# Kernel optimization log

Hardware: AMD Instinct MI355X
Metric: run time of the kernel (lower is better)

## Reference

```python
import jax, jax.numpy as jnp
import numpy as np

# Mamba2 hyperparams fixed by MambaBlock.__init__ (d_model=512, d_state=128, d_conv=4, expand=4, headdim=64)
D_MODEL = 512
D_STATE = 128      # N
D_CONV = 4
EXPAND = 4
HEADDIM = 64       # P
D_INNER = EXPAND * D_MODEL            # 2048
NHEADS = D_INNER // HEADDIM           # 32
NGROUPS = 1
CONV_DIM = D_INNER + 2 * NGROUPS * D_STATE      # 2304 (x, B, C share the depthwise conv)
D_IN_PROJ = 2 * D_INNER + 2 * NGROUPS * D_STATE + NHEADS  # 4384 (z, xBC, dt)
EPS = 1e-5


def _mamba2(x, in_w, conv_w, conv_b, dt_bias, A_log, Dp, norm_w, out_w):
    """Faithful Mamba2 forward (ngroups=1). x: [B, L, d_model]."""
    Bsz, L, _ = x.shape
    zxbcdt = jnp.einsum('bld,pd->blp', x, in_w)  # in_proj (no bias)
    z, xBC, dt = jnp.split(zxbcdt, [D_INNER, D_INNER + CONV_DIM], axis=-1)
    # causal depthwise conv1d over xBC, kernel size D_CONV, then SiLU
    xp = jnp.pad(xBC, ((0, 0), (D_CONV - 1, 0), (0, 0)))
    xBC = sum(xp[:, k:k + L, :] * conv_w[:, k] for k in range(D_CONV)) + conv_b
    xBC = jax.nn.silu(xBC)
    xs, Bc, Cc = jnp.split(xBC, [D_INNER, D_INNER + D_STATE], axis=-1)
    xs = xs.reshape(Bsz, L, NHEADS, HEADDIM)          # [B,L,H,P]
    dt = jax.nn.softplus(dt + dt_bias)                 # [B,L,H]
    A = -jnp.exp(A_log)                                # [H]
    dA = jnp.exp(dt * A)                               # [B,L,H] discrete state decay

    def step(h, inp):
        dA_t, dt_t, x_t, B_t, C_t = inp  # [B,H],[B,H],[B,H,P],[B,N],[B,N]
        h = h * dA_t[:, :, None, None] + (dt_t[:, :, None] * x_t)[..., None] * B_t[:, None, None, :]
        y = jnp.einsum('bhpn,bn->bhp', h, C_t)
        return h, y

    h0 = jnp.zeros((Bsz, NHEADS, HEADDIM, D_STATE), x.dtype)
    inps = (dA.transpose(1, 0, 2), dt.transpose(1, 0, 2), xs.transpose(1, 0, 2, 3),
            Bc.transpose(1, 0, 2), Cc.transpose(1, 0, 2))
    _, ys = jax.lax.scan(step, h0, inps)               # [L,B,H,P]
    y = ys.transpose(1, 0, 2, 3) + Dp[None, None, :, None] * xs  # skip via D
    y = y.reshape(Bsz, L, D_INNER)
    # RMSNormGated (norm_before_gate=False): gate first, then RMSNorm
    y = y * jax.nn.silu(z)
    y = y * jax.lax.rsqrt(jnp.mean(y * y, axis=-1, keepdims=True) + EPS) * norm_w
    return jnp.einsum('bld,od->blo', y, out_w)         # out_proj (no bias)


def _make_params(key):
    ks = jax.random.split(key, 8)
    return dict(
        in_w=jax.random.normal(ks[0], (D_IN_PROJ, D_MODEL), jnp.float32) / np.sqrt(D_MODEL),
        conv_w=jax.random.normal(ks[1], (CONV_DIM, D_CONV), jnp.float32) * 0.2,
        conv_b=jax.random.normal(ks[2], (CONV_DIM,), jnp.float32) * 0.02,
        dt_bias=jax.random.normal(ks[3], (NHEADS,), jnp.float32) * 0.1,
        A_log=jnp.log(jax.random.uniform(ks[4], (NHEADS,), jnp.float32, 1.0, 16.0)),
        D=jnp.ones((NHEADS,), jnp.float32),
        norm_w=jnp.ones((D_INNER,), jnp.float32),
        out_w=jax.random.normal(ks[5], (D_MODEL, D_INNER), jnp.float32) / np.sqrt(D_INNER),
    )


def setup_inputs() -> dict:
    key = jax.random.key(0)
    k_in, k_f, k_b = jax.random.split(key, 3)
    x = jax.random.normal(k_in, (2, 2048, D_MODEL), jnp.float32)
    pf = _make_params(k_f)
    pb = _make_params(k_b)
    out = {'input': x}
    for n, v in pf.items():
        out['f_' + n] = v
    for n, v in pb.items():
        out['b_' + n] = v
    return out


def reference(input, f_in_w, f_conv_w, f_conv_b, f_dt_bias, f_A_log, f_D, f_norm_w, f_out_w,
              b_in_w, b_conv_w, b_conv_b, b_dt_bias, b_A_log, b_D, b_norm_w, b_out_w):
    fwd = _mamba2(input, f_in_w, f_conv_w, f_conv_b, f_dt_bias, f_A_log, f_D, f_norm_w, f_out_w)
    xb = jnp.flip(input, axis=1)
    bwd = _mamba2(xb, b_in_w, b_conv_w, b_conv_b, b_dt_bias, b_A_log, b_D, b_norm_w, b_out_w)
    bwd = jnp.flip(bwd, axis=1)
    return jnp.concatenate([fwd + input, bwd + input], axis=-1)
```

## Files before the change

### kernel.cpp

```cpp
#include <hip/hip_runtime.h>
#include <hip/hip_bf16.h>
#include <math.h>

#define L_SEQ   2048
#define M_ROWS  4096
#define DPROJ   4384
#define DPROJP  4480
#define NPROJ   4352
#define DINNER  2048
#define CONVDIM 2304
#define NST     128
#define NH      32
#define CHUNK   128
#define NCH     16
#define CTR     32
#define NTILE   (L_SEQ / CTR)
#define LOG2E   1.4426950408889634f

typedef __attribute__((ext_vector_type(8))) short short8;
typedef __attribute__((ext_vector_type(4))) float f32x4;
typedef unsigned short u16;

static __device__ __forceinline__ u16 bf16bits(float v) {
    __hip_bfloat16 t = __float2bfloat16(v);
    return *(u16*)&t;
}
static __device__ __forceinline__ float bits2f(u16 u) {
    return __uint_as_float((unsigned)u << 16);
}
static __device__ __forceinline__ int sidx(int row, int s) {
    return (row << 7) + ((((s >> 3) ^ (row & 7)) << 3) | (s & 7));
}
static __device__ __forceinline__ int sslot(int row, int ks) {
    return (row << 7) + ((ks ^ (row & 7)) << 3);
}
static __device__ __forceinline__ void gload16(const void* g, void* l) {
    __builtin_amdgcn_global_load_lds(
        (const __attribute__((address_space(1))) void*)g,
        (__attribute__((address_space(3))) void*)l, 16, 0, 0);
}

__global__ __launch_bounds__(256) void cvt_x_kernel(
    const float* __restrict__ x, u16* __restrict__ xbf)
{
    const int i = (blockIdx.x * 256 + threadIdx.x) * 4;
    const float4 v = *(const float4*)(x + i);
    xbf[i + 0] = bf16bits(v.x);
    xbf[i + 1] = bf16bits(v.y);
    xbf[i + 2] = bf16bits(v.z);
    xbf[i + 3] = bf16bits(v.w);
}

__global__ __launch_bounds__(256) void cvt_win_kernel(
    const float* __restrict__ w0, const float* __restrict__ w1,
    u16* __restrict__ dst)
{
    const int dir = blockIdx.y;
    const float* __restrict__ w = dir ? w1 : w0;
    u16* __restrict__ d = dst + (size_t)dir * NPROJ * 512;
    const int i = (blockIdx.x * 256 + threadIdx.x) * 4;
    const float4 v = *(const float4*)(w + i);
    d[i + 0] = bf16bits(v.x);
    d[i + 1] = bf16bits(v.y);
    d[i + 2] = bf16bits(v.z);
    d[i + 3] = bf16bits(v.w);
}

__global__ __launch_bounds__(256) void cvt_wout_kernel(
    const float* __restrict__ w0, const float* __restrict__ w1,
    u16* __restrict__ dst)
{
    const int dir = blockIdx.y;
    const float* __restrict__ w = dir ? w1 : w0;
    u16* __restrict__ d = dst + (size_t)dir * 512 * DINNER;
    const int i = (blockIdx.x * 256 + threadIdx.x) * 4;
    const float4 v = *(const float4*)(w + i);
    d[i + 0] = bf16bits(v.x);
    d[i + 1] = bf16bits(v.y);
    d[i + 2] = bf16bits(v.z);
    d[i + 3] = bf16bits(v.w);
}

__global__ __launch_bounds__(256) void gemm_mfma_in(
    const u16* __restrict__ A0, int lda,
    const u16* __restrict__ Bw, long long b_dir_off,
    u16* __restrict__ Cb, long long c_dir_off, int ldc,
    int K)
{
    const int dir = blockIdx.z;
    const int nwg  = gridDim.x * gridDim.y;
    const int flat = blockIdx.y * gridDim.x + blockIdx.x;
    const int q = nwg >> 3, r = nwg & 7;
    const int xcd = flat & 7, idx = flat >> 3;
    const int wg = (xcd < r) ? xcd * (q + 1) + idx
                             : r * (q + 1) + (xcd - r) * q + idx;
    const int m0 = (wg / gridDim.x) * 128;
    const int n0 = (wg % gridDim.x) * 128;

    const u16* __restrict__ A = A0;
    const u16* __restrict__ B = Bw + (size_t)dir * b_dir_off;

    __shared__ u16 Asl[128 * 64];
    __shared__ u16 Bsl[128 * 64];

    const int tid  = threadIdx.x;
    const int lane = tid & 63;
    const int wid  = tid >> 6;
    const int wr   = (wid >> 1) << 6;
    const int wc   = (wid & 1) << 6;
    const int l15  = lane & 15;
    const int l4   = lane >> 4;

    f32x4 acc[4][4];
#pragma unroll
    for (int m = 0; m < 4; ++m)
#pragma unroll
        for (int n = 0; n < 4; ++n) acc[m][n] = (f32x4)0.f;

    for (int k0 = 0; k0 < K; k0 += 64) {
        __syncthreads();
#pragma unroll
        for (int i = 0; i < 4; ++i) {
            const int c    = tid + (i << 8);
            const int row  = c >> 3;
            const int scol = ((c & 7) ^ (row & 7)) << 3;
            gload16(A + (size_t)(m0 + row) * lda + k0 + scol, (char*)Asl + (c << 4));
            gload16(B + (size_t)(n0 + row) * K   + k0 + scol, (char*)Bsl + (c << 4));
        }
        __syncthreads();

#pragma unroll
        for (int kh = 0; kh < 2; ++kh) {
            const int ks = (kh << 2) + l4;
            short8 a[4], b[4];
#pragma unroll
            for (int m = 0; m < 4; ++m) {
                const int R = wr + (m << 4) + l15;
                a[m] = *(const short8*)((const char*)Asl + (R << 7) + ((ks ^ (R & 7)) << 4));
            }
#pragma unroll
            for (int n = 0; n < 4; ++n) {
                const int R = wc + (n << 4) + l15;
                b[n] = *(const short8*)((const char*)Bsl + (R << 7) + ((ks ^ (R & 7)) << 4));
            }
#pragma unroll
            for (int m = 0; m < 4; ++m)
#pragma unroll
                for (int n = 0; n < 4; ++n)
                    acc[m][n] = __builtin_amdgcn_mfma_f32_16x16x32_bf16(
                        a[m], b[n], acc[m][n], 0, 0, 0);
        }
    }

#pragma unroll
    for (int m = 0; m < 4; ++m) {
        const int row0 = m0 + wr + (m << 4) + (l4 << 2);
#pragma unroll
        for (int n = 0; n < 4; ++n) {
            const int col = n0 + wc + (n << 4) + l15;
#pragma unroll
            for (int r2 = 0; r2 < 4; ++r2)
                Cb[(size_t)dir * c_dir_off + (size_t)(row0 + r2) * ldc + col] =
                    bf16bits(acc[m][n][r2]);
        }
    }
}

__global__ __launch_bounds__(256) void gemm_out_kernel(
    const u16* __restrict__ Azx,
    const u16* __restrict__ Bw,
    const float* __restrict__ x,
    float* __restrict__ out)
{
    const int dir = blockIdx.z;
    const int nwg  = gridDim.x * gridDim.y;
    const int flat = blockIdx.y * gridDim.x + blockIdx.x;
    const int q = nwg >> 3;
    const int xcd = flat & 7, idx = flat >> 3;
    const int wg = xcd * q + idx;
    const int m0 = (wg >> 3) * 128;
    const int n0 = (wg & 7) * 64;

    const u16* __restrict__ A = Azx + (size_t)dir * M_ROWS * DPROJP + DINNER;
    const u16* __restrict__ B = Bw + (size_t)dir * 512 * DINNER;

    __shared__ u16 Asl[128 * 64];
    __shared__ u16 Bsl[64 * 64];

    const int tid  = threadIdx.x;
    const int lane = tid & 63;
    const int wid  = tid >> 6;
    const int wr   = (wid >> 1) << 6;
    const int wc   = (wid & 1) << 5;
    const int l15  = lane & 15;
    const int l4   = lane >> 4;

    f32x4 acc[4][2];
#pragma unroll
    for (int m = 0; m < 4; ++m)
#pragma unroll
        for (int n = 0; n < 2; ++n) acc[m][n] = (f32x4)0.f;

    for (int k0 = 0; k0 < DINNER; k0 += 64) {
        __syncthreads();
#pragma unroll
        for (int i = 0; i < 4; ++i) {
            const int c    = tid + (i << 8);
            const int row  = c >> 3;
            const int scol = ((c & 7) ^ (row & 7)) << 3;
            gload16(A + (size_t)(m0 + row) * DPROJP + k0 + scol, (char*)Asl + (c << 4));
        }
#pragma unroll
        for (int i = 0; i < 2; ++i) {
            const int c    = tid + (i << 8);
            const int row  = c >> 3;
            const int scol = ((c & 7) ^ (row & 7)) << 3;
            gload16(B + (size_t)(n0 + row) * DINNER + k0 + scol, (char*)Bsl + (c << 4));
        }
        __syncthreads();

#pragma unroll
        for (int kh = 0; kh < 2; ++kh) {
            const int ks = (kh << 2) + l4;
            short8 a[4], b[2];
#pragma unroll
            for (int m = 0; m < 4; ++m) {
                const int R = wr + (m << 4) + l15;
                a[m] = *(const short8*)((const char*)Asl + (R << 7) + ((ks ^ (R & 7)) << 4));
            }
#pragma unroll
            for (int n = 0; n < 2; ++n) {
                const int R = wc + (n << 4) + l15;
                b[n] = *(const short8*)((const char*)Bsl + (R << 7) + ((ks ^ (R & 7)) << 4));
            }
#pragma unroll
            for (int m = 0; m < 4; ++m)
#pragma unroll
                for (int n = 0; n < 2; ++n)
                    acc[m][n] = __builtin_amdgcn_mfma_f32_16x16x32_bf16(
                        a[m], b[n], acc[m][n], 0, 0, 0);
        }
    }

#pragma unroll
    for (int m = 0; m < 4; ++m) {
        const int row0 = m0 + wr + (m << 4) + (l4 << 2);
#pragma unroll
        for (int n = 0; n < 2; ++n) {
            const int col = n0 + wc + (n << 4) + l15;
#pragma unroll
            for (int r2 = 0; r2 < 4; ++r2) {
                const float v = acc[m][n][r2] + x[(size_t)(row0 + r2) * 512 + col];
                out[(size_t)(row0 + r2) * 1024 + dir * 512 + col] = v;
            }
        }
    }
}

__global__ __launch_bounds__(256) void conv_kernel(
    const u16* __restrict__ zx,
    const float* __restrict__ cw0, const float* __restrict__ cw1,
    const float* __restrict__ cb0, const float* __restrict__ cb1,
    u16* __restrict__ xs, u16* __restrict__ Bbf, u16* __restrict__ Cbf)
{
    const int dir = blockIdx.z;
    const int c   = blockIdx.x * 256 + threadIdx.x;
    const int b   = blockIdx.y >> 6;
    const int r0  = (blockIdx.y & (NTILE - 1)) * CTR;

    const float* __restrict__ cw = dir ? cw1 : cw0;
    const float w0 = cw[c * 4 + 0], w1 = cw[c * 4 + 1];
    const float w2 = cw[c * 4 + 2], w3 = cw[c * 4 + 3];
    const float bias = (dir ? cb1 : cb0)[c];

    const u16* __restrict__ zcol = zx + (size_t)dir * M_ROWS * DPROJP
        + (size_t)(b * L_SEQ) * DPROJP + DINNER + c;
    const size_t obase = (size_t)(dir * M_ROWS + b * L_SEQ);

    auto emit = [&](int l, float acc) {
        const float s = acc / (1.f + expf(-acc));
        const size_t orow = obase + l;
        if (c < DINNER)            xs[orow * DINNER + c] = bf16bits(s);
        else if (c < DINNER + NST) Bbf[orow * NST + (c - DINNER)] = bf16bits(s);
        else                       Cbf[orow * NST + (c - DINNER - NST)] = bf16bits(s);
    };

    if (dir == 0) {
        float h0 = (r0 - 3 >= 0) ? bits2f(zcol[(size_t)(r0 - 3) * DPROJP]) : 0.f;
        float h1 = (r0 - 2 >= 0) ? bits2f(zcol[(size_t)(r0 - 2) * DPROJP]) : 0.f;
        float h2 = (r0 - 1 >= 0) ? bits2f(zcol[(size_t)(r0 - 1) * DPROJP]) : 0.f;
#pragma unroll 8
        for (int l = r0; l < r0 + CTR; ++l) {
            const float zl = bits2f(zcol[(size_t)l * DPROJP]);
            float acc = bias;
            acc = fmaf(w0, h0, acc);
            acc = fmaf(w1, h1, acc);
            acc = fmaf(w2, h2, acc);
            acc = fmaf(w3, zl, acc);
            emit(l, acc);
            h0 = h1; h1 = h2; h2 = zl;
        }
    } else {
        const int le = r0 + CTR - 1;
        float h1 = (le + 1 < L_SEQ) ? bits2f(zcol[(size_t)(le + 1) * DPROJP]) : 0.f;
        float h2 = (le + 2 < L_SEQ) ? bits2f(zcol[(size_t)(le + 2) * DPROJP]) : 0.f;
        float h3 = (le + 3 < L_SEQ) ? bits2f(zcol[(size_t)(le + 3) * DPROJP]) : 0.f;
#pragma unroll 8
        for (int l = le; l >= r0; --l) {
            const float zl = bits2f(zcol[(size_t)l * DPROJP]);
            float acc = bias;
            acc = fmaf(w3, zl, acc);
            acc = fmaf(w2, h1, acc);
            acc = fmaf(w1, h2, acc);
            acc = fmaf(w0, h3, acc);
            emit(l, acc);
            h3 = h2; h2 = h1; h1 = zl;
        }
    }
}

__global__ __launch_bounds__(512) void dt_kernel(
    const float* __restrict__ x,
    const float* __restrict__ inw0, const float* __restrict__ inw1,
    const float* __restrict__ dtbias0, const float* __restrict__ dtbias1,
    const float* __restrict__ Alog0, const float* __restrict__ Alog1,
    float* __restrict__ dtb, float* __restrict__ dta)
{
    const int dir = blockIdx.y;
    const int r0  = blockIdx.x * 64;
    const int tid = threadIdx.x;

    __shared__ float wT[512 * 32];
    __shared__ float sbias[NH], sa[NH];

    const float* __restrict__ w = (dir ? inw1 : inw0) + (size_t)(DINNER + CONVDIM) * 512;
    for (int i = tid; i < 4096; i += 512) {
        const int flat = i * 4;
        const int h = flat >> 9;
        const int k = flat & 511;
        const float4 v = *(const float4*)(w + flat);
        *(float4*)&wT[(k >> 2) * 128 + h * 4] = v;
    }
    if (tid < NH) {
        sbias[tid] = (dir ? dtbias1 : dtbias0)[tid];
        sa[tid] = -expf((dir ? Alog1 : Alog0)[tid]) * LOG2E;
    }
    __syncthreads();

    const int h  = tid & 31;
    const int rr = tid >> 5;
    const float bias = sbias[h];
    const float a = sa[h];

    for (int rp = 0; rp < 64; rp += 16) {
        const int row = r0 + rp + rr;
        const float4* __restrict__ xr = (const float4*)(x + (size_t)row * 512);
        float4 s4 = make_float4(0.f, 0.f, 0.f, 0.f);
#pragma unroll 8
        for (int k4 = 0; k4 < 128; ++k4) {
            const float4 xv = xr[k4];
            const float4 wv = *(const float4*)&wT[k4 * 128 + h * 4];
            s4.x = fmaf(xv.x, wv.x, s4.x);
            s4.y = fmaf(xv.y, wv.y, s4.y);
            s4.z = fmaf(xv.z, wv.z, s4.z);
            s4.w = fmaf(xv.w, wv.w, s4.w);
        }
        const float v = (s4.x + s4.y) + (s4.z + s4.w) + bias;
        const float sp = (v > 20.f) ? v : log1pf(expf(v));
        const size_t orow = (size_t)(dir * M_ROWS + row);
        dtb[orow * NH + h] = sp;
        dta[orow * NH + h] = sp * a;
    }
}

__global__ __launch_bounds__(256) void sraw_kernel(
    const u16* __restrict__ Bbf, const u16* __restrict__ Cbf,
    u16* __restrict__ Sraw)
{
    const int bx  = blockIdx.x;
    const int ch  = bx & (NCH - 1);
    const int db  = bx >> 4;
    const int dir = db >> 1, bb = db & 1;
    const int tid = threadIdx.x;
    const int wid = tid >> 6;
    const int lane = tid & 63;
    const int l15 = lane & 15, l4 = lane >> 4;
    const int t0  = ch * CHUNK;
    const size_t dbase = (size_t)(dir * M_ROWS + bb * L_SEQ);
    const size_t base  = ((size_t)bx) << 14;

    auto lidx = [&](int t) { return dir ? (L_SEQ - 1 - t) : t; };

    f32x4 accs[2][8];
#pragma unroll
    for (int m = 0; m < 2; ++m)
#pragma unroll
        for (int j = 0; j < 8; ++j) accs[m][j] = (f32x4)0.f;

    short8 af[2][4];
#pragma unroll
    for (int m = 0; m < 2; ++m) {
        const size_t crow = dbase + lidx(t0 + wid * 32 + m * 16 + l15);
#pragma unroll
        for (int kk = 0; kk < 4; ++kk)
            af[m][kk] = *(const short8*)(Cbf + crow * NST + kk * 32 + l4 * 8);
    }
#pragma unroll
    for (int j = 0; j < 8; ++j) {
        const size_t brow = dbase + lidx(t0 + j * 16 + l15);
        short8 bf_[4];
#pragma unroll
        for (int kk = 0; kk < 4; ++kk)
            bf_[kk] = *(const short8*)(Bbf + brow * NST + kk * 32 + l4 * 8);
#pragma unroll
        for (int m = 0; m < 2; ++m)
#pragma unroll
            for (int kk = 0; kk < 4; ++kk)
                accs[m][j] = __builtin_amdgcn_mfma_f32_16x16x32_bf16(
                    af[m][kk], bf_[kk], accs[m][j], 0, 0, 0);
    }

#pragma unroll
    for (int m = 0; m < 2; ++m)
#pragma unroll
        for (int j = 0; j < 8; ++j)
#pragma unroll
            for (int r = 0; r < 4; ++r) {
                const int t = wid * 32 + m * 16 + l4 * 4 + r;
                const int s = j * 16 + l15;
                Sraw[base + (size_t)t * 128 + s] = bf16bits(accs[m][j][r]);
            }
}

__global__ __launch_bounds__(512) void ssd_state_kernel(
    const u16* __restrict__ xs, const u16* __restrict__ Bbf,
    const float* __restrict__ dtb, const float* __restrict__ dta,
    u16* __restrict__ stateC, float* __restrict__ betac)
{
    const int bx  = blockIdx.x;
    const int ch  = bx & (NCH - 1);
    const int bh  = bx >> 4;
    const int dir = bh >> 6;
    const int bb  = (bh >> 5) & 1;
    const int h   = bh & 31;
    const int tid = threadIdx.x;
    const int wid = tid >> 6;
    const int lane = tid & 63;
    const int l15 = lane & 15;
    const int l4  = lane >> 4;
    const int t0  = ch * CHUNK;
    const size_t dbase = (size_t)(dir * M_ROWS + bb * L_SEQ);

    __shared__ u16 XT[64 * 128];
    __shared__ u16 WBT[128 * 128];
    __shared__ float scum[CHUNK];
    __shared__ float sdt[CHUNK];

    auto lidx = [&](int t) { return dir ? (L_SEQ - 1 - t) : t; };

    const int sP = tid >> 2;
    const size_t grow = dbase + lidx(t0 + sP);
    const int p0 = (tid & 3) * 16;
    const int n0 = (tid & 3) * 32;
    short8 xv[2], bv[4];
#pragma unroll
    for (int q = 0; q < 2; ++q)
        xv[q] = *(const short8*)(xs + grow * DINNER + h * 64 + p0 + q * 8);
#pragma unroll
    for (int q = 0; q < 4; ++q)
        bv[q] = *(const short8*)(Bbf + grow * NST + n0 + q * 8);

    if (tid >= 128 && tid < 256) {
        const int s = tid - 128;
        sdt[s] = dtb[(dbase + lidx(t0 + s)) * NH + h];
    }
    if (wid == 0) {
        float a0 = dta[(dbase + lidx(t0 + lane)) * NH + h];
        float a1 = dta[(dbase + lidx(t0 + 64 + lane)) * NH + h];
#pragma unroll
        for (int off = 1; off < 64; off <<= 1) {
            const float u0 = __shfl_up(a0, off);
            const float u1 = __shfl_up(a1, off);
            if (lane >= off) { a0 += u0; a1 += u1; }
        }
        a1 += __shfl(a0, 63);
        scum[lane] = a0; scum[64 + lane] = a1;
        betac[(size_t)bh * L_SEQ + t0 + lane] = a0;
        betac[(size_t)bh * L_SEQ + t0 + 64 + lane] = a1;
    }
    __syncthreads();

    {
        const float dts = sdt[sP];
        const float rs  = exp2f(scum[CHUNK - 1] - scum[sP]);
#pragma unroll
        for (int q = 0; q < 2; ++q)
#pragma unroll
            for (int j = 0; j < 8; ++j)
                XT[sidx(p0 + q * 8 + j, sP)] = bf16bits(dts * bits2f((u16)xv[q][j]));
#pragma unroll
        for (int q = 0; q < 4; ++q)
#pragma unroll
            for (int j = 0; j < 8; ++j)
                WBT[sidx(n0 + q * 8 + j, sP)] = bf16bits(rs * bits2f((u16)bv[q][j]));
    }
    __syncthreads();

    const int pw = (wid >> 1) << 4;
    const int nh = (wid & 1) << 6;
    const int prow = pw + l15;
    short8 xa[4];
#pragma unroll
    for (int kk = 0; kk < 4; ++kk)
        xa[kk] = *(const short8*)(XT + sslot(prow, kk * 4 + l4));
    const size_t sbase = ((size_t)bh * NCH + ch) * 8192;
#pragma unroll
    for (int jn = 0; jn < 4; ++jn) {
        const int nrow = nh + jn * 16 + l15;
        f32x4 acc = (f32x4)0.f;
#pragma unroll
        for (int kk = 0; kk < 4; ++kk) {
            const short8 wb = *(const short8*)(WBT + sslot(nrow, kk * 4 + l4));
            acc = __builtin_amdgcn_mfma_f32_16x16x32_bf16(xa[kk], wb, acc, 0, 0, 0);
        }
#pragma unroll
        for (int r = 0; r < 4; ++r)
            stateC[sbase + (size_t)(pw + l4 * 4 + r) * 128 + nh + jn * 16 + l15] =
                bf16bits(acc[r]);
    }
}

__global__ __launch_bounds__(512) void combine_kernel(
    u16* __restrict__ stateC, const float* __restrict__ betac)
{
    const int bh  = blockIdx.x;
    const int tid = threadIdx.x;

    float hrun[16];
#pragma unroll
    for (int j = 0; j < 16; ++j) hrun[j] = 0.f;

    for (int s = 0; s < NCH; ++s) {
        const size_t off = ((size_t)bh * NCH + s) * 8192 + (size_t)tid * 16;
        float c[16];
#pragma unroll
        for (int j = 0; j < 16; ++j) c[j] = bits2f(stateC[off + j]);
#pragma unroll
        for (int j = 0; j < 16; ++j) stateC[off + j] = bf16bits(hrun[j]);
        const float alpha = exp2f(betac[(size_t)bh * L_SEQ + s * CHUNK + (CHUNK - 1)]);
#pragma unroll
        for (int j = 0; j < 16; ++j) hrun[j] = fmaf(alpha, hrun[j], c[j]);
    }
}

__global__ __launch_bounds__(512) void ssd_out_kernel(
    const u16* __restrict__ xs, const u16* __restrict__ Cbf,
    const u16* __restrict__ Sraw, const u16* __restrict__ stateC,
    const float* __restrict__ dtb, const float* __restrict__ betac,
    const float* __restrict__ D0, const float* __restrict__ D1,
    u16* __restrict__ yb)
{
    const int bx  = blockIdx.x;
    const int ch  = bx & (NCH - 1);
    const int bh  = bx >> 4;
    const int dir = bh >> 6;
    const int bb  = (bh >> 5) & 1;
    const int h   = bh & 31;
    const int tid = threadIdx.x;
    const int wid = tid >> 6;
    const int lane = tid & 63;
    const int l15 = lane & 15;
    const int l4  = lane >> 4;
    const int t0  = ch * CHUNK;
    const size_t dbase = (size_t)(dir * M_ROWS + bb * L_SEQ);
    const float Dv = (dir ? D1 : D0)[h];

    __shared__ u16 XT[64 * 128];
    __shared__ u16 HS[64 * 128];
    __shared__ float scum[CHUNK];
    __shared__ float sdt[CHUNK];

    auto lidx = [&](int t) { return dir ? (L_SEQ - 1 - t) : t; };

    const int trow = wid * 16 + l15;
    const size_t sbraw = ((size_t)(((bh >> 5) * NCH) + ch)) << 14;
    const size_t crow = dbase + lidx(t0 + trow);
    const size_t sbase = ((size_t)bh * NCH + ch) * 8192;

    short8 sv[4], c8[4];
#pragma unroll
    for (int kk = 0; kk < 4; ++kk) {
        const int sb = kk * 32 + l4 * 8;
        sv[kk] = *(const short8*)(Sraw + sbraw + (size_t)trow * 128 + sb);
        c8[kk] = *(const short8*)(Cbf + crow * NST + sb);
    }
    u16 xsv[16];
#pragma unroll
    for (int jp = 0; jp < 4; ++jp)
#pragma unroll
        for (int r = 0; r < 4; ++r) {
            const int t = wid * 16 + l4 * 4 + r;
            xsv[jp * 4 + r] =
                xs[(dbase + lidx(t0 + t)) * DINNER + h * 64 + jp * 16 + l15];
        }

#pragma unroll
    for (int i = 0; i < 2; ++i) {
        const int c = tid + (i << 9);
        const int row = c >> 4;
        const int sl  = c & 15;
        *(short8*)(HS + sslot(row, sl)) =
            *(const short8*)(stateC + sbase + (size_t)row * 128 + sl * 8);
    }
    if (tid < 128) {
        scum[tid] = betac[(size_t)bh * L_SEQ + t0 + tid];
    } else if (tid < 256) {
        const int s = tid - 128;
        sdt[s] = dtb[(dbase + lidx(t0 + s)) * NH + h];
    }
    __syncthreads();

    {
        const int s = tid >> 2;
        const float dts = sdt[s];
        const size_t grow = dbase + lidx(t0 + s);
        const int p0 = (tid & 3) * 16;
        const u16* __restrict__ xp = xs + grow * DINNER + h * 64 + p0;
#pragma unroll
        for (int q = 0; q < 2; ++q) {
            short8 v = *(const short8*)(xp + q * 8);
#pragma unroll
            for (int j = 0; j < 8; ++j) {
                const int p = p0 + q * 8 + j;
                XT[sidx(p, s)] = bf16bits(dts * bits2f((u16)v[j]));
            }
        }
    }
    __syncthreads();

    u16* __restrict__ ybase = yb + (size_t)dir * M_ROWS * DINNER;

    const float ct = scum[trow];
    const float gs = exp2f(ct);
    short8 pa[4], ga[4];
#pragma unroll
    for (int kk = 0; kk < 4; ++kk) {
        const int sb = kk * 32 + l4 * 8;
        short8 o, og;
#pragma unroll
        for (int j = 0; j < 8; ++j) {
            const float g = ((sb + j) <= trow) ? exp2f(ct - scum[sb + j]) : 0.f;
            o[j]  = (short)bf16bits(bits2f((u16)sv[kk][j]) * g);
            og[j] = (short)bf16bits(bits2f((u16)c8[kk][j]) * gs);
        }
        pa[kk] = o;
        ga[kk] = og;
    }

#pragma unroll
    for (int jp = 0; jp < 4; ++jp) {
        const int prow = jp * 16 + l15;
        short8 xb[4], hb[4];
#pragma unroll
        for (int kk = 0; kk < 4; ++kk) {
            xb[kk] = *(const short8*)(XT + sslot(prow, kk * 4 + l4));
            hb[kk] = *(const short8*)(HS + sslot(prow, kk * 4 + l4));
        }
        f32x4 acc = (f32x4)0.f;
#pragma unroll
        for (int kk = 0; kk < 4; ++kk)
            acc = __builtin_amdgcn_mfma_f32_16x16x32_bf16(
                pa[kk], xb[kk], acc, 0, 0, 0);
#pragma unroll
        for (int kk = 0; kk < 4; ++kk)
            acc = __builtin_amdgcn_mfma_f32_16x16x32_bf16(
                ga[kk], hb[kk], acc, 0, 0, 0);
#pragma unroll
        for (int r = 0; r < 4; ++r) {
            const int t = wid * 16 + l4 * 4 + r;
            const int lg = lidx(t0 + t);
            const float xv = bits2f(xsv[jp * 4 + r]);
            ybase[(size_t)(bb * L_SEQ + lg) * DINNER + h * 64 + prow] =
                bf16bits(acc[r] + Dv * xv);
        }
    }
}

__global__ __launch_bounds__(256) void gatenorm_kernel(
    u16* __restrict__ zx, const u16* __restrict__ yb,
    const float* __restrict__ nw0, const float* __restrict__ nw1)
{
    const int dir = blockIdx.y;
    const int row = blockIdx.x;
    const float* __restrict__ nw = dir ? nw1 : nw0;
    u16* __restrict__ zrow = zx + (size_t)dir * M_ROWS * DPROJP + (size_t)row * DPROJP;
    const u16* __restrict__ yrow = yb + (size_t)dir * M_ROWS * DINNER + (size_t)row * DINNER;
    const int tid = threadIdx.x;
    const int c0 = tid * 8;

    const short8 zv = *(const short8*)(zrow + c0);
    const short8 yv8 = *(const short8*)(yrow + c0);

    float g[8];
#pragma unroll
    for (int j = 0; j < 8; ++j) {
        const float z = bits2f((u16)zv[j]);
        g[j] = bits2f((u16)yv8[j]) * (z / (1.f + expf(-z)));
    }

    float ss = 0.f;
#pragma unroll
    for (int j = 0; j < 8; ++j) ss = fmaf(g[j], g[j], ss);
#pragma unroll
    for (int off = 1; off < 64; off <<= 1) ss += __shfl_xor(ss, off);
    __shared__ float red[4];
    if ((tid & 63) == 0) red[tid >> 6] = ss;
    __syncthreads();
    const float total = red[0] + red[1] + red[2] + red[3];
    const float rs = rsqrtf(total * (1.f / (float)DINNER) + 1e-5f);

    const float4 w0 = *(const float4*)(nw + c0);
    const float4 w1 = *(const float4*)(nw + c0 + 4);
    const float wv[8] = {w0.x, w0.y, w0.z, w0.w, w1.x, w1.y, w1.z, w1.w};
    short8 outv;
#pragma unroll
    for (int j = 0; j < 8; ++j) outv[j] = (short)bf16bits(g[j] * rs * wv[j]);
    *(short8*)(zrow + DINNER + c0) = outv;
}

extern "C" void kernel_launch(void* const* d_in, const int* in_sizes, int n_in,
                              void* d_out, int out_size, void* d_ws, size_t ws_size,
                              hipStream_t stream)
{
    (void)in_sizes; (void)n_in; (void)out_size; (void)ws_size;
    const float* x        = (const float*)d_in[0];
    const float* f_in_w   = (const float*)d_in[1];
    const float* f_conv_w = (const float*)d_in[2];
    const float* f_conv_b = (const float*)d_in[3];
    const float* f_dtbias = (const float*)d_in[4];
    const float* f_Alog   = (const float*)d_in[5];
    const float* f_D      = (const float*)d_in[6];
    const float* f_nw     = (const float*)d_in[7];
    const float* f_out_w  = (const float*)d_in[8];
    const float* b_in_w   = (const float*)d_in[9];
    const float* b_conv_w = (const float*)d_in[10];
    const float* b_conv_b = (const float*)d_in[11];
    const float* b_dtbias = (const float*)d_in[12];
    const float* b_Alog   = (const float*)d_in[13];
    const float* b_D      = (const float*)d_in[14];
    const float* b_nw     = (const float*)d_in[15];
    const float* b_out_w  = (const float*)d_in[16];

    u16* zx  = (u16*)d_ws;
    u16* xs  = zx + (size_t)2 * M_ROWS * DPROJP;
    u16* Bbf = xs + (size_t)2 * M_ROWS * DINNER;
    u16* Cbf = Bbf + (size_t)2 * M_ROWS * NST;
    float* dtb = (float*)(Cbf + (size_t)2 * M_ROWS * NST);
    float* dta = dtb + (size_t)2 * M_ROWS * NH;
    u16* stateC = (u16*)(dta + (size_t)2 * M_ROWS * NH);
    float* betac = (float*)(stateC + (size_t)128 * NCH * 8192);
    u16* yb = (u16*)(betac + (size_t)128 * L_SEQ);
    u16* x_bf   = yb + (size_t)2 * M_ROWS * DINNER;
    u16* w_in_bf  = x_bf + (size_t)M_ROWS * 512;
    u16* w_out_bf = w_in_bf + (size_t)2 * DPROJP * 512;
    u16* Sraw = w_out_bf + (size_t)2 * 512 * DINNER;

    cvt_x_kernel<<<dim3(M_ROWS * 512 / 1024), 256, 0, stream>>>(x, x_bf);
    cvt_win_kernel<<<dim3(NPROJ * 512 / 1024, 2), 256, 0, stream>>>(f_in_w, b_in_w, w_in_bf);
    cvt_wout_kernel<<<dim3(512 * DINNER / 1024, 2), 256, 0, stream>>>(f_out_w, b_out_w, w_out_bf);

    gemm_mfma_in<<<dim3(NPROJ / 128, M_ROWS / 128, 2), 256, 0, stream>>>(
        x_bf, 512,
        w_in_bf, (long long)NPROJ * 512,
        zx, (long long)M_ROWS * DPROJP, DPROJP,
        512);

    conv_kernel<<<dim3(CONVDIM / 256, 2 * NTILE, 2), 256, 0, stream>>>(
        zx, f_conv_w, b_conv_w, f_conv_b, b_conv_b, xs, Bbf, Cbf);

    dt_kernel<<<dim3(M_ROWS / 64, 2), 512, 0, stream>>>(
        x, f_in_w, b_in_w, f_dtbias, b_dtbias, f_Alog, b_Alog, dtb, dta);

    sraw_kernel<<<dim3(4 * NCH), 256, 0, stream>>>(Bbf, Cbf, Sraw);

    ssd_state_kernel<<<dim3(128 * NCH), 512, 0, stream>>>(
        xs, Bbf, dtb, dta, stateC, betac);

    combine_kernel<<<dim3(128), 512, 0, stream>>>(stateC, betac);

    ssd_out_kernel<<<dim3(128 * NCH), 512, 0, stream>>>(
        xs, Cbf, Sraw, stateC, dtb, betac, f_D, b_D, yb);

    gatenorm_kernel<<<dim3(M_ROWS, 2), 256, 0, stream>>>(zx, yb, f_nw, b_nw);

    gemm_out_kernel<<<dim3(8, 32, 2), 256, 0, stream>>>(
        zx, w_out_bf, x, (float*)d_out);
}
```

Measured before the change: 263.9 us.

## Fuse gating into SSD output, fold norm weight into out_proj, apply rsqrt in epilogue

Result: no change. 260.3 us (-1.3%).

```diff
diff --git a/kernel.cpp b/kernel.cpp
--- a/kernel.cpp
+++ b/kernel.cpp
@@ -68,17 +68,20 @@
 
 __global__ __launch_bounds__(256) void cvt_wout_kernel(
     const float* __restrict__ w0, const float* __restrict__ w1,
+    const float* __restrict__ nw0, const float* __restrict__ nw1,
     u16* __restrict__ dst)
 {
     const int dir = blockIdx.y;
     const float* __restrict__ w = dir ? w1 : w0;
+    const float* __restrict__ nw = dir ? nw1 : nw0;
     u16* __restrict__ d = dst + (size_t)dir * 512 * DINNER;
     const int i = (blockIdx.x * 256 + threadIdx.x) * 4;
+    const int k = i & (DINNER - 1);
     const float4 v = *(const float4*)(w + i);
-    d[i + 0] = bf16bits(v.x);
-    d[i + 1] = bf16bits(v.y);
-    d[i + 2] = bf16bits(v.z);
-    d[i + 3] = bf16bits(v.w);
+    d[i + 0] = bf16bits(v.x * nw[k + 0]);
+    d[i + 1] = bf16bits(v.y * nw[k + 1]);
+    d[i + 2] = bf16bits(v.z * nw[k + 2]);
+    d[i + 3] = bf16bits(v.w * nw[k + 3]);
 }
 
 __global__ __launch_bounds__(256) void gemm_mfma_in(
@@ -167,8 +170,9 @@
 }
 
 __global__ __launch_bounds__(256) void gemm_out_kernel(
-    const u16* __restrict__ Azx,
+    const u16* __restrict__ Ag,
     const u16* __restrict__ Bw,
+    const float* __restrict__ rs,
     const float* __restrict__ x,
     float* __restrict__ out)
 {
@@ -181,8 +185,9 @@
     const int m0 = (wg >> 3) * 128;
     const int n0 = (wg & 7) * 64;
 
-    const u16* __restrict__ A = Azx + (size_t)dir * M_ROWS * DPROJP + DINNER;
+    const u16* __restrict__ A = Ag + (size_t)dir * M_ROWS * DINNER;
     const u16* __restrict__ B = Bw + (size_t)dir * 512 * DINNER;
+    const float* __restrict__ rsd = rs + (size_t)dir * M_ROWS;
 
     __shared__ u16 Asl[128 * 64];
     __shared__ u16 Bsl[64 * 64];
@@ -208,7 +213,7 @@
             const int c    = tid + (i << 8);
             const int row  = c >> 3;
             const int scol = ((c & 7) ^ (row & 7)) << 3;
-            gload16(A + (size_t)(m0 + row) * DPROJP + k0 + scol, (char*)Asl + (c << 4));
+            gload16(A + (size_t)(m0 + row) * DINNER + k0 + scol, (char*)Asl + (c << 4));
         }
 #pragma unroll
         for (int i = 0; i < 2; ++i) {
@@ -250,7 +255,8 @@
             const int col = n0 + wc + (n << 4) + l15;
 #pragma unroll
             for (int r2 = 0; r2 < 4; ++r2) {
-                const float v = acc[m][n][r2] + x[(size_t)(row0 + r2) * 512 + col];
+                const float v = acc[m][n][r2] * rsd[row0 + r2]
+                              + x[(size_t)(row0 + r2) * 512 + col];
                 out[(size_t)(row0 + r2) * 1024 + dir * 512 + col] = v;
             }
         }
@@ -556,6 +562,7 @@
 __global__ __launch_bounds__(512) void ssd_out_kernel(
     const u16* __restrict__ xs, const u16* __restrict__ Cbf,
     const u16* __restrict__ Sraw, const u16* __restrict__ stateC,
+    const u16* __restrict__ zx,
     const float* __restrict__ dtb, const float* __restrict__ betac,
     const float* __restrict__ D0, const float* __restrict__ D1,
     u16* __restrict__ yb)
@@ -594,14 +601,15 @@
         sv[kk] = *(const short8*)(Sraw + sbraw + (size_t)trow * 128 + sb);
         c8[kk] = *(const short8*)(Cbf + crow * NST + sb);
     }
-    u16 xsv[16];
+    u16 xsv[16], zsv[16];
 #pragma unroll
     for (int jp = 0; jp < 4; ++jp)
 #pragma unroll
         for (int r = 0; r < 4; ++r) {
             const int t = wid * 16 + l4 * 4 + r;
-            xsv[jp * 4 + r] =
-                xs[(dbase + lidx(t0 + t)) * DINNER + h * 64 + jp * 16 + l15];
+            const size_t gr = dbase + lidx(t0 + t);
+            xsv[jp * 4 + r] = xs[gr * DINNER + h * 64 + jp * 16 + l15];
+            zsv[jp * 4 + r] = zx[gr * DPROJP + h * 64 + jp * 16 + l15];
         }
 
 #pragma unroll
@@ -679,53 +687,39 @@
         for (int r = 0; r < 4; ++r) {
             const int t = wid * 16 + l4 * 4 + r;
             const int lg = lidx(t0 + t);
-            const float xv = bits2f(xsv[jp * 4 + r]);
-            ybase[(size_t)(bb * L_SEQ + lg) * DINNER + h * 64 + prow] =
-                bf16bits(acc[r] + Dv * xv);
-        }
-    }
-}
-
-__global__ __launch_bounds__(256) void gatenorm_kernel(
-    u16* __restrict__ zx, const u16* __restrict__ yb,
-    const float* __restrict__ nw0, const float* __restrict__ nw1)
+            const float yv = acc[r] + Dv * bits2f(xsv[jp * 4 + r]);
+            const float zz = bits2f(zsv[jp * 4 + r]);
+            const float g  = yv * (zz / (1.f + expf(-zz)));
+            ybase[(size_t)(bb * L_SEQ + lg) * DINNER + h * 64 + prow] = bf16bits(g);
+        }
+    }
+}
+
+__global__ __launch_bounds__(256) void rs_kernel(
+    const u16* __restrict__ yb, float* __restrict__ rs)
 {
     const int dir = blockIdx.y;
     const int row = blockIdx.x;
-    const float* __restrict__ nw = dir ? nw1 : nw0;
-    u16* __restrict__ zrow = zx + (size_t)dir * M_ROWS * DPROJP + (size_t)row * DPROJP;
-    const u16* __restrict__ yrow = yb + (size_t)dir * M_ROWS * DINNER + (size_t)row * DINNER;
+    const u16* __restrict__ yrow = yb + ((size_t)dir * M_ROWS + row) * DINNER;
     const int tid = threadIdx.x;
-    const int c0 = tid * 8;
-
-    const short8 zv = *(const short8*)(zrow + c0);
-    const short8 yv8 = *(const short8*)(yrow + c0);
-
-    float g[8];
+
+    const short8 yv8 = *(const short8*)(yrow + tid * 8);
+    float ss = 0.f;
 #pragma unroll
     for (int j = 0; j < 8; ++j) {
-        const float z = bits2f((u16)zv[j]);
-        g[j] = bits2f((u16)yv8[j]) * (z / (1.f + expf(-z)));
-    }
-
-    float ss = 0.f;
-#pragma unroll
-    for (int j = 0; j < 8; ++j) ss = fmaf(g[j], g[j], ss);
+        const float g = bits2f((u16)yv8[j]);
+        ss = fmaf(g, g, ss);
+    }
 #pragma unroll
     for (int off = 1; off < 64; off <<= 1) ss += __shfl_xor(ss, off);
     __shared__ float red[4];
     if ((tid & 63) == 0) red[tid >> 6] = ss;
     __syncthreads();
-    const float total = red[0] + red[1] + red[2] + red[3];
-    const float rs = rsqrtf(total * (1.f / (float)DINNER) + 1e-5f);
-
-    const float4 w0 = *(const float4*)(nw + c0);
-    const float4 w1 = *(const float4*)(nw + c0 + 4);
-    const float wv[8] = {w0.x, w0.y, w0.z, w0.w, w1.x, w1.y, w1.z, w1.w};
-    short8 outv;
-#pragma unroll
-    for (int j = 0; j < 8; ++j) outv[j] = (short)bf16bits(g[j] * rs * wv[j]);
-    *(short8*)(zrow + DINNER + c0) = outv;
+    if (tid == 0) {
+        const float total = red[0] + red[1] + red[2] + red[3];
+        rs[(size_t)dir * M_ROWS + row] =
+            rsqrtf(total * (1.f / (float)DINNER) + 1e-5f);
+    }
 }
 
 extern "C" void kernel_launch(void* const* d_in, const int* in_sizes, int n_in,
@@ -764,10 +758,12 @@
     u16* w_in_bf  = x_bf + (size_t)M_ROWS * 512;
     u16* w_out_bf = w_in_bf + (size_t)2 * DPROJP * 512;
     u16* Sraw = w_out_bf + (size_t)2 * 512 * DINNER;
+    float* rsbuf = (float*)(Sraw + (size_t)64 * 128 * 128);
 
     cvt_x_kernel<<<dim3(M_ROWS * 512 / 1024), 256, 0, stream>>>(x, x_bf);
     cvt_win_kernel<<<dim3(NPROJ * 512 / 1024, 2), 256, 0, stream>>>(f_in_w, b_in_w, w_in_bf);
-    cvt_wout_kernel<<<dim3(512 * DINNER / 1024, 2), 256, 0, stream>>>(f_out_w, b_out_w, w_out_bf);
+    cvt_wout_kernel<<<dim3(512 * DINNER / 1024, 2), 256, 0, stream>>>(
+        f_out_w, b_out_w, f_nw, b_nw, w_out_bf);
 
     gemm_mfma_in<<<dim3(NPROJ / 128, M_ROWS / 128, 2), 256, 0, stream>>>(
         x_bf, 512,
@@ -789,10 +785,10 @@
     combine_kernel<<<dim3(128), 512, 0, stream>>>(stateC, betac);
 
     ssd_out_kernel<<<dim3(128 * NCH), 512, 0, stream>>>(
-        xs, Cbf, Sraw, stateC, dtb, betac, f_D, b_D, yb);
-
-    gatenorm_kernel<<<dim3(M_ROWS, 2), 256, 0, stream>>>(zx, yb, f_nw, b_nw);
+        xs, Cbf, Sraw, stateC, zx, dtb, betac, f_D, b_D, yb);
+
+    rs_kernel<<<dim3(M_ROWS, 2), 256, 0, stream>>>(yb, rsbuf);
 
     gemm_out_kernel<<<dim3(8, 32, 2), 256, 0, stream>>>(
-        zx, w_out_bf, x, (float*)d_out);
-}
+        yb, w_out_bf, rsbuf, x, (float*)d_out);
+}
```
